# Kernel optimization log

Hardware: AMD Instinct MI355X
Metric: run time of the kernel (lower is better)

The kernel has to match this reference:

```python
import jax, jax.numpy as jnp
import numpy as np

B, C, T = 128, 9, 2048
R = T // 4            # reduced_timesteps after two MaxPool1d(2)
N = B * R             # total graph nodes
E_SINGLE = 8192       # edges per sample graph (avg degree 16 over R nodes)
HID = 128
OUT = 12


def setup_inputs():
    key = jax.random.key(0)
    ks = jax.random.split(key, 14)
    x = jax.random.normal(ks[0], (B, C, T), jnp.float32)
    # per-sample graph, replicated with offset i*R per batch element (as in forward)
    single = jax.random.randint(ks[1], (2, E_SINGLE), 0, R)
    offsets = (jnp.arange(B) * R)[None, :, None]
    edge_index = (single[:, None, :] + offsets).reshape(2, -1)  # [2, B*E_SINGLE]

    def lin(k, fan_in, shape):
        return jax.random.normal(k, shape, jnp.float32) / np.sqrt(fan_in)

    return {
        "x": x,
        "edge_index": edge_index,
        "conv1_w": lin(ks[2], C * 5, (16, C, 5)),
        "conv1_b": jnp.zeros((16,), jnp.float32),
        "conv2_w": lin(ks[3], 16 * 5, (32, 16, 5)),
        "conv2_b": jnp.zeros((32,), jnp.float32),
        "gcn1_w": lin(ks[4], 32, (32, HID)),
        "gcn1_b": jnp.zeros((HID,), jnp.float32),
        "gcn2_w": lin(ks[5], HID, (HID, HID)),
        "gcn2_b": jnp.zeros((HID,), jnp.float32),
        "fc_w": lin(ks[6], HID, (HID, OUT)),
        "fc_b": jnp.zeros((OUT,), jnp.float32),
    }


def _gcn_conv(h, edge_index, w, b, n):
    # PyG GCNConv: linear -> add self-loops -> sym-normalized sum aggregation -> + bias
    h = h @ w
    loops = jnp.arange(n)
    row = jnp.concatenate([edge_index[0], loops])  # source
    col = jnp.concatenate([edge_index[1], loops])  # target (aggregation)
    deg = jax.ops.segment_sum(jnp.ones(col.shape, h.dtype), col, num_segments=n)
    dis = jnp.where(deg > 0, jax.lax.rsqrt(jnp.maximum(deg, 1e-12)), 0.0)
    norm = dis[row] * dis[col]                      # [E+N]
    out = jax.ops.segment_sum(norm[:, None] * h[row], col, num_segments=n)
    return out + b


def _temporal_conv(x, w1, b1, w2, b2):
    dn = ("NCH", "OIH", "NCH")
    h = jax.lax.conv_general_dilated(x, w1, (1,), [(2, 2)], dimension_numbers=dn)
    h = jax.nn.relu(h + b1[None, :, None])
    h = jax.lax.reduce_window(h, -jnp.inf, jax.lax.max, (1, 1, 2), (1, 1, 2), "VALID")
    h = jax.lax.conv_general_dilated(h, w2, (1,), [(2, 2)], dimension_numbers=dn)
    h = jax.nn.relu(h + b2[None, :, None])
    h = jax.lax.reduce_window(h, -jnp.inf, jax.lax.max, (1, 1, 2), (1, 1, 2), "VALID")
    return h  # [B, 32, R]


def reference(x, edge_index, conv1_w, conv1_b, conv2_w, conv2_b,
              gcn1_w, gcn1_b, gcn2_w, gcn2_b, fc_w, fc_b):
    h = _temporal_conv(x, conv1_w, conv1_b, conv2_w, conv2_b)   # [B, 32, R]
    nodes = h.transpose(0, 2, 1).reshape(B * R, 32)             # [N, 32]
    g = jax.nn.relu(_gcn_conv(nodes, edge_index, gcn1_w, gcn1_b, N))
    g = jax.nn.relu(_gcn_conv(g, edge_index, gcn2_w, gcn2_b, N))
    g = g.reshape(B, R, HID).mean(axis=1)                       # [B, HID]
    return g @ fc_w + fc_b                                      # [B, OUT]
```

## Files before the change

kernel.cpp:

```cpp
#include <hip/hip_runtime.h>
#include <hip/hip_bf16.h>

#define BB   128
#define CIN  9
#define TT   2048
#define RR   512
#define NN   (BB*RR)
#define HID  128
#define NOUT 12

typedef __attribute__((ext_vector_type(8))) short short8;
typedef __attribute__((ext_vector_type(4))) float f32x4;

static __device__ inline unsigned short f2bf(float f) {
    unsigned int u = __float_as_uint(f);
    unsigned int r = (u + 0x7fffu + ((u >> 16) & 1u)) >> 16;
    return (unsigned short)r;
}
static __device__ inline float bf2f(unsigned short u) {
    return __uint_as_float(((unsigned int)u) << 16);
}

__global__ __launch_bounds__(512) void k_convs(const float* __restrict__ x,
        const float* __restrict__ w1, const float* __restrict__ b1,
        const float* __restrict__ w2, const float* __restrict__ b2,
        float* __restrict__ nodes,
        const int* __restrict__ ei, int E, int es,
        int* __restrict__ rptr, float* __restrict__ dis, int* __restrict__ adj) {
    __shared__ float sx[CIN][268];
    __shared__ float s1[16][132];
    __shared__ int lcnt[512];
    __shared__ int sp[512];
    __shared__ int lcur[512];
    int tid = threadIdx.x;

    if (blockIdx.x == 1024) {
        int t = tid;
        lcnt[t] = 0;
        __syncthreads();
        for (int i = t; i < es; i += 512) atomicAdd(&lcnt[ei[E + i]], 1);
        __syncthreads();
        int c = lcnt[t];
        sp[t] = c;
        __syncthreads();
        for (int off = 1; off < 512; off <<= 1) {
            int v = sp[t];
            int add = (t >= off) ? sp[t - off] : 0;
            __syncthreads();
            sp[t] = v + add;
            __syncthreads();
        }
        int excl = sp[t] - c;
        rptr[t] = excl;
        if (t == 511) rptr[512] = es;
        dis[t] = rsqrtf((float)c + 1.0f);
        lcur[t] = excl;
        __syncthreads();
        for (int i = t; i < es; i += 512) {
            int row = ei[i], col = ei[E + i];
            int pos = atomicAdd(&lcur[col], 1);
            adj[pos] = row;
        }
        return;
    }

    int b  = blockIdx.x >> 3;
    int r0 = (blockIdx.x & 7) * 64;
    int wv   = __builtin_amdgcn_readfirstlane(tid >> 6);
    int lane = tid & 63;

    for (int idx = tid; idx < CIN * 268; idx += 512) {
        int c = idx / 268, j = idx - c * 268;
        int g = 4 * r0 - 6 + j;
        float v = 0.f;
        if (g >= 0 && g < TT) v = x[(b * CIN + c) * TT + g];
        sx[c][j] = v;
    }
    __syncthreads();

#pragma unroll
    for (int cc = 0; cc < 2; ++cc) {
        int c1 = wv * 2 + cc;
        float bias1 = b1[c1];
        for (int pp = lane; pp < 132; pp += 64) {
            int p = 2 * r0 - 2 + pp;
            float val = 0.f;
            if (p >= 0 && p < 1024) {
                float a0 = bias1, a1 = bias1;
#pragma unroll
                for (int c = 0; c < CIN; ++c) {
                    const float2* px = (const float2*)&sx[c][2 * pp];
                    float2 q0 = px[0], q1 = px[1], q2 = px[2];
                    const float* wp = &w1[(c1 * CIN + c) * 5];
                    float k0 = wp[0], k1 = wp[1], k2 = wp[2], k3 = wp[3], k4 = wp[4];
                    a0 += q0.x*k0 + q0.y*k1 + q1.x*k2 + q1.y*k3 + q2.x*k4;
                    a1 += q0.y*k0 + q1.x*k1 + q1.y*k2 + q2.x*k3 + q2.y*k4;
                }
                val = fmaxf(fmaxf(a0, a1), 0.f);
            }
            s1[c1][pp] = val;
        }
    }
    __syncthreads();

    int rl = lane;
    float acc0[4], acc1[4];
#pragma unroll
    for (int o = 0; o < 4; ++o) {
        float bv = b2[wv * 4 + o];
        acc0[o] = bv; acc1[o] = bv;
    }
#pragma unroll
    for (int c = 0; c < 16; ++c) {
        const float2* ps = (const float2*)&s1[c][2 * rl];
        float2 q0 = ps[0], q1 = ps[1], q2 = ps[2];
#pragma unroll
        for (int o = 0; o < 4; ++o) {
            const float* wp = &w2[((wv * 4 + o) * 16 + c) * 5];
            float k0 = wp[0], k1 = wp[1], k2 = wp[2], k3 = wp[3], k4 = wp[4];
            acc0[o] += q0.x*k0 + q0.y*k1 + q1.x*k2 + q1.y*k3 + q2.x*k4;
            acc1[o] += q0.y*k0 + q1.x*k1 + q1.y*k2 + q2.x*k3 + q2.y*k4;
        }
    }
    int n = b * RR + r0 + rl;
    float4 ov;
    ov.x = fmaxf(fmaxf(acc0[0], acc1[0]), 0.f);
    ov.y = fmaxf(fmaxf(acc0[1], acc1[1]), 0.f);
    ov.z = fmaxf(fmaxf(acc0[2], acc1[2]), 0.f);
    ov.w = fmaxf(fmaxf(acc0[3], acc1[3]), 0.f);
    *(float4*)&nodes[n * 32 + wv * 4] = ov;
}

__global__ __launch_bounds__(256) void k_gl1(const int* __restrict__ rptr,
        const int* __restrict__ adj, const float* __restrict__ dis,
        const float* __restrict__ nodes, const float* __restrict__ w,
        const float* __restrict__ bias, unsigned short* __restrict__ h16) {
    __shared__ float srow[32][32];
    __shared__ float sw[32 * 128];
    int bid = (blockIdx.x & 7) * 256 + (blockIdx.x >> 3);
    int tid = threadIdx.x;
    int nbase = bid * 32;
    int b = nbase >> 9;
    const float* hb = nodes + (size_t)b * RR * 32;

    {
        const float4* src = (const float4*)w;
        float4* dst = (float4*)sw;
#pragma unroll
        for (int i = 0; i < 4; ++i) dst[tid + i * 256] = src[tid + i * 256];
    }

    int ln   = tid >> 3;
    int lane = tid & 7;
    int r = (nbase & 511) + ln;
    int s = rptr[r], e = rptr[r + 1];
    float dn = dis[r];
    float4 acc = make_float4(0.f, 0.f, 0.f, 0.f);
    for (int base = s; base < e; base += 8) {
        int j = base + lane;
        int src = 0; float nd = 0.f;
        if (j < e) { src = adj[j]; nd = dis[src]; }
        int cnt = min(8, e - base);
        int k = 0;
        for (; k + 4 <= cnt; k += 4) {
            int   s0 = __shfl(src, k, 8),     s1 = __shfl(src, k + 1, 8);
            int   s2 = __shfl(src, k + 2, 8), s3 = __shfl(src, k + 3, 8);
            float n0 = __shfl(nd, k, 8),      n1 = __shfl(nd, k + 1, 8);
            float n2 = __shfl(nd, k + 2, 8),  n3 = __shfl(nd, k + 3, 8);
            float4 v0 = *(const float4*)&hb[(size_t)s0 * 32 + lane * 4];
            float4 v1 = *(const float4*)&hb[(size_t)s1 * 32 + lane * 4];
            float4 v2 = *(const float4*)&hb[(size_t)s2 * 32 + lane * 4];
            float4 v3 = *(const float4*)&hb[(size_t)s3 * 32 + lane * 4];
            float w0 = dn * n0, w1 = dn * n1, w2 = dn * n2, w3 = dn * n3;
            acc.x += w0*v0.x + w1*v1.x + w2*v2.x + w3*v3.x;
            acc.y += w0*v0.y + w1*v1.y + w2*v2.y + w3*v3.y;
            acc.z += w0*v0.z + w1*v1.z + w2*v2.z + w3*v3.z;
            acc.w += w0*v0.w + w1*v1.w + w2*v2.w + w3*v3.w;
        }
        for (; k < cnt; ++k) {
            int   sk = __shfl(src, k, 8);
            float nk = __shfl(nd, k, 8);
            float4 v = *(const float4*)&hb[(size_t)sk * 32 + lane * 4];
            float wgt = dn * nk;
            acc.x += wgt * v.x; acc.y += wgt * v.y;
            acc.z += wgt * v.z; acc.w += wgt * v.w;
        }
    }
    {
        float4 v = *(const float4*)&hb[(size_t)r * 32 + lane * 4];
        float wgt = dn * dn;
        acc.x += wgt * v.x; acc.y += wgt * v.y;
        acc.z += wgt * v.z; acc.w += wgt * v.w;
    }
    *(float4*)&srow[ln][lane * 4] = acc;
    __syncthreads();

    int fq = tid & 31;
    int ng = tid >> 5;
    float a[4][4];
#pragma unroll
    for (int j = 0; j < 4; ++j)
#pragma unroll
        for (int q = 0; q < 4; ++q) a[j][q] = 0.f;
#pragma unroll
    for (int c = 0; c < 32; ++c) {
        float4 wvv = *(const float4*)&sw[c * 128 + fq * 4];
#pragma unroll
        for (int j = 0; j < 4; ++j) {
            float xc = srow[ng * 4 + j][c];
            a[j][0] += xc * wvv.x; a[j][1] += xc * wvv.y;
            a[j][2] += xc * wvv.z; a[j][3] += xc * wvv.w;
        }
    }
    float4 bv = *(const float4*)&bias[fq * 4];
#pragma unroll
    for (int j = 0; j < 4; ++j) {
        ushort4 o;
        o.x = f2bf(fmaxf(a[j][0] + bv.x, 0.f));
        o.y = f2bf(fmaxf(a[j][1] + bv.y, 0.f));
        o.z = f2bf(fmaxf(a[j][2] + bv.z, 0.f));
        o.w = f2bf(fmaxf(a[j][3] + bv.w, 0.f));
        *(ushort4*)&h16[(size_t)(nbase + ng * 4 + j) * 128 + fq * 4] = o;
    }
}

__global__ __launch_bounds__(256) void k_lin2(const unsigned short* __restrict__ g16,
        const float* __restrict__ w, unsigned short* __restrict__ h16) {
    __shared__ unsigned short srow[64][136];
    __shared__ unsigned short swT[128][136];
    int tid = threadIdx.x;
    int nbase = blockIdx.x * 64;

    {
        const ushort4* src = (const ushort4*)(g16 + (size_t)nbase * 128);
#pragma unroll
        for (int i = 0; i < 8; ++i) {
            int idx = tid + i * 256;
            int row = idx >> 5, col4 = idx & 31;
            ushort4 v = src[idx];
            *(ushort4*)&srow[row][col4 * 4] = v;
        }
    }
    {
        for (int i = 0; i < 64; ++i) {
            int idx = i * 256 + tid;
            int c = idx >> 7, f = idx & 127;
            swT[f][c] = f2bf(w[idx]);
        }
    }
    __syncthreads();

    int wv  = tid >> 6;
    int lane = tid & 63;
    int m0 = wv * 16;
    int l15 = lane & 15;
    int quad = lane >> 4;
    f32x4 acc[8];
#pragma unroll
    for (int nt = 0; nt < 8; ++nt) acc[nt] = (f32x4){0.f, 0.f, 0.f, 0.f};
#pragma unroll
    for (int kc = 0; kc < 4; ++kc) {
        int k0 = kc * 32 + quad * 8;
        short8 a = *(const short8*)&srow[m0 + l15][k0];
#pragma unroll
        for (int nt = 0; nt < 8; ++nt) {
            short8 b = *(const short8*)&swT[nt * 16 + l15][k0];
            acc[nt] = __builtin_amdgcn_mfma_f32_16x16x32_bf16(a, b, acc[nt], 0, 0, 0);
        }
    }
#pragma unroll
    for (int nt = 0; nt < 8; ++nt) {
#pragma unroll
        for (int r = 0; r < 4; ++r) {
            int row = m0 + quad * 4 + r;
            int col = nt * 16 + l15;
            h16[(size_t)(nbase + row) * 128 + col] = f2bf(acc[nt][r]);
        }
    }
}

__global__ __launch_bounds__(256) void k_gather128(const int* __restrict__ rptr,
        const int* __restrict__ adj, const float* __restrict__ dis,
        const unsigned short* __restrict__ h, const float* __restrict__ bias,
        float* __restrict__ partial) {
    __shared__ float sred[8][128];
    int bid  = (blockIdx.x & 7) * 1024 + (blockIdx.x >> 3);
    int tid  = threadIdx.x;
    int g    = tid >> 5;
    int lane = tid & 31;
    int node = bid * 8 + g;
    int b = node >> 9;
    int r = node & 511;
    const unsigned short* hb = h + (size_t)b * RR * 128;
    int s = rptr[r], e = rptr[r + 1];
    float dn = dis[r];
    float4 acc = make_float4(0.f, 0.f, 0.f, 0.f);
    for (int base = s; base < e; base += 32) {
        int j = base + lane;
        int src = 0; float nd = 0.f;
        if (j < e) { src = adj[j]; nd = dis[src]; }
        int cnt = min(32, e - base);
        int k = 0;
        for (; k + 4 <= cnt; k += 4) {
            int   s0 = __shfl(src, k, 32),     s1 = __shfl(src, k + 1, 32);
            int   s2 = __shfl(src, k + 2, 32), s3 = __shfl(src, k + 3, 32);
            float n0 = __shfl(nd, k, 32),      n1 = __shfl(nd, k + 1, 32);
            float n2 = __shfl(nd, k + 2, 32),  n3 = __shfl(nd, k + 3, 32);
            ushort4 u0 = *(const ushort4*)&hb[(size_t)s0 * 128 + lane * 4];
            ushort4 u1 = *(const ushort4*)&hb[(size_t)s1 * 128 + lane * 4];
            ushort4 u2 = *(const ushort4*)&hb[(size_t)s2 * 128 + lane * 4];
            ushort4 u3 = *(const ushort4*)&hb[(size_t)s3 * 128 + lane * 4];
            float w0 = dn * n0, w1 = dn * n1, w2 = dn * n2, w3 = dn * n3;
            acc.x += w0*bf2f(u0.x) + w1*bf2f(u1.x) + w2*bf2f(u2.x) + w3*bf2f(u3.x);
            acc.y += w0*bf2f(u0.y) + w1*bf2f(u1.y) + w2*bf2f(u2.y) + w3*bf2f(u3.y);
            acc.z += w0*bf2f(u0.z) + w1*bf2f(u1.z) + w2*bf2f(u2.z) + w3*bf2f(u3.z);
            acc.w += w0*bf2f(u0.w) + w1*bf2f(u1.w) + w2*bf2f(u2.w) + w3*bf2f(u3.w);
        }
        for (; k < cnt; ++k) {
            int   sk = __shfl(src, k, 32);
            float nk = __shfl(nd, k, 32);
            ushort4 u = *(const ushort4*)&hb[(size_t)sk * 128 + lane * 4];
            float wgt = dn * nk;
            acc.x += wgt * bf2f(u.x); acc.y += wgt * bf2f(u.y);
            acc.z += wgt * bf2f(u.z); acc.w += wgt * bf2f(u.w);
        }
    }
    ushort4 u = *(const ushort4*)&hb[(size_t)r * 128 + lane * 4];
    float wgt = dn * dn;
    float4 bv = *(const float4*)&bias[lane * 4];
    acc.x = fmaxf(acc.x + wgt * bf2f(u.x) + bv.x, 0.f);
    acc.y = fmaxf(acc.y + wgt * bf2f(u.y) + bv.y, 0.f);
    acc.z = fmaxf(acc.z + wgt * bf2f(u.z) + bv.z, 0.f);
    acc.w = fmaxf(acc.w + wgt * bf2f(u.w) + bv.w, 0.f);
    *(float4*)&sred[g][lane * 4] = acc;
    __syncthreads();
    if (tid < 128) {
        float ssum = 0.f;
#pragma unroll
        for (int j = 0; j < 8; ++j) ssum += sred[j][tid];
        partial[(size_t)bid * 128 + tid] = ssum;
    }
}

__global__ __launch_bounds__(128) void k_fc(const float* __restrict__ partial,
        const float* __restrict__ fw, const float* __restrict__ fb,
        float* __restrict__ out) {
    __shared__ float sm[HID];
    int b = blockIdx.x, f = threadIdx.x;
    float acc = 0.f;
#pragma unroll 8
    for (int j = 0; j < 64; ++j) acc += partial[(size_t)(b * 64 + j) * 128 + f];
    sm[f] = acc * (1.0f / RR);
    __syncthreads();
    if (f < NOUT) {
        float s = fb[f];
#pragma unroll
        for (int c = 0; c < HID; ++c) s += sm[c] * fw[c * NOUT + f];
        out[b * NOUT + f] = s;
    }
}

extern "C" void kernel_launch(void* const* d_in, const int* in_sizes, int n_in,
                              void* d_out, int out_size, void* d_ws, size_t ws_size,
                              hipStream_t stream) {
    const float* x   = (const float*)d_in[0];
    const int*   ei  = (const int*)d_in[1];
    const float* c1w = (const float*)d_in[2];
    const float* c1b = (const float*)d_in[3];
    const float* c2w = (const float*)d_in[4];
    const float* c2b = (const float*)d_in[5];
    const float* g1w = (const float*)d_in[6];
    const float* g1b = (const float*)d_in[7];
    const float* g2w = (const float*)d_in[8];
    const float* g2b = (const float*)d_in[9];
    const float* fw  = (const float*)d_in[10];
    const float* fb  = (const float*)d_in[11];
    float* out = (float*)d_out;
    int E  = in_sizes[1] / 2;
    int es = E / BB;

    char* ws = (char*)d_ws;
    float*          nodes   = (float*)(ws);
    unsigned short* bufA16  = (unsigned short*)(ws + (8u  << 20));
    unsigned short* bufC16  = (unsigned short*)(ws + (24u << 20));
    int*   rptr    = (int*)  (ws + (40u << 20));
    float* dis     = (float*)(ws + (40u << 20) + 4096);
    int*   adj     = (int*)  (ws + (40u << 20) + 8192);
    float* partial = (float*)(ws + (41u << 20));

    k_convs<<<BB * 8 + 1, 512, 0, stream>>>(x, c1w, c1b, c2w, c2b, nodes,
                                            ei, E, es, rptr, dis, adj);

    k_gl1<<<NN / 32, 256, 0, stream>>>(rptr, adj, dis, nodes, g1w, g1b, bufA16);

    k_lin2<<<NN / 64, 256, 0, stream>>>(bufA16, g2w, bufC16);
    k_gather128<<<NN / 8, 256, 0, stream>>>(rptr, adj, dis, bufC16, g2b, partial);

    k_fc<<<BB, 128, 0, stream>>>(partial, fw, fb, out);
}
```

Before: 176.0 us.

## Stage per-sample graph in LDS, fuse layer-2 linear with gather, use MFMA

```diff
diff --git a/kernel.cpp b/kernel.cpp
--- a/kernel.cpp
+++ b/kernel.cpp
@@ -26,7 +26,9 @@
         const float* __restrict__ w2, const float* __restrict__ b2,
         float* __restrict__ nodes,
         const int* __restrict__ ei, int E, int es,
-        int* __restrict__ rptr, float* __restrict__ dis, int* __restrict__ adj) {
+        int* __restrict__ rptr, float* __restrict__ dis, int* __restrict__ adj,
+        const float* __restrict__ g1w, const float* __restrict__ g2w,
+        unsigned short* __restrict__ w1t, unsigned short* __restrict__ w2t) {
     __shared__ float sx[CIN][268];
     __shared__ float s1[16][132];
     __shared__ int lcnt[512];
@@ -63,6 +65,17 @@
         }
         return;
     }
+    if (blockIdx.x == 1025) {
+        for (int idx = tid; idx < 32 * 128; idx += 512) {
+            int c = idx >> 7, f = idx & 127;
+            w1t[f * 32 + c] = f2bf(g1w[idx]);
+        }
+        for (int idx = tid; idx < 128 * 128; idx += 512) {
+            int c = idx >> 7, f = idx & 127;
+            w2t[f * 128 + c] = f2bf(g2w[idx]);
+        }
+        return;
+    }
 
     int b  = blockIdx.x >> 3;
     int r0 = (blockIdx.x & 7) * 64;
@@ -131,214 +144,226 @@
     *(float4*)&nodes[n * 32 + wv * 4] = ov;
 }
 
-__global__ __launch_bounds__(256) void k_gl1(const int* __restrict__ rptr,
+__global__ __launch_bounds__(512, 2) void k_gl1(const int* __restrict__ rptr,
         const int* __restrict__ adj, const float* __restrict__ dis,
-        const float* __restrict__ nodes, const float* __restrict__ w,
+        const float* __restrict__ nodes, const unsigned short* __restrict__ w1t,
         const float* __restrict__ bias, unsigned short* __restrict__ h16) {
-    __shared__ float srow[32][32];
-    __shared__ float sw[32 * 128];
-    int bid = (blockIdx.x & 7) * 256 + (blockIdx.x >> 3);
+    __shared__ float snode[512][36];
+    __shared__ unsigned short srow[256][40];
+    __shared__ float sdis[512];
     int tid = threadIdx.x;
-    int nbase = bid * 32;
-    int b = nbase >> 9;
-    const float* hb = nodes + (size_t)b * RR * 32;
+    int vb = blockIdx.x;
+    int xcd = vb & 7, slot = vb >> 3;
+    int b = xcd * 16 + (slot >> 1);
+    int half = slot & 1;
 
     {
-        const float4* src = (const float4*)w;
-        float4* dst = (float4*)sw;
-#pragma unroll
-        for (int i = 0; i < 4; ++i) dst[tid + i * 256] = src[tid + i * 256];
-    }
-
-    int ln   = tid >> 3;
-    int lane = tid & 7;
-    int r = (nbase & 511) + ln;
-    int s = rptr[r], e = rptr[r + 1];
-    float dn = dis[r];
-    float4 acc = make_float4(0.f, 0.f, 0.f, 0.f);
-    for (int base = s; base < e; base += 8) {
-        int j = base + lane;
-        int src = 0; float nd = 0.f;
-        if (j < e) { src = adj[j]; nd = dis[src]; }
-        int cnt = min(8, e - base);
-        int k = 0;
-        for (; k + 4 <= cnt; k += 4) {
-            int   s0 = __shfl(src, k, 8),     s1 = __shfl(src, k + 1, 8);
-            int   s2 = __shfl(src, k + 2, 8), s3 = __shfl(src, k + 3, 8);
-            float n0 = __shfl(nd, k, 8),      n1 = __shfl(nd, k + 1, 8);
-            float n2 = __shfl(nd, k + 2, 8),  n3 = __shfl(nd, k + 3, 8);
-            float4 v0 = *(const float4*)&hb[(size_t)s0 * 32 + lane * 4];
-            float4 v1 = *(const float4*)&hb[(size_t)s1 * 32 + lane * 4];
-            float4 v2 = *(const float4*)&hb[(size_t)s2 * 32 + lane * 4];
-            float4 v3 = *(const float4*)&hb[(size_t)s3 * 32 + lane * 4];
-            float w0 = dn * n0, w1 = dn * n1, w2 = dn * n2, w3 = dn * n3;
-            acc.x += w0*v0.x + w1*v1.x + w2*v2.x + w3*v3.x;
-            acc.y += w0*v0.y + w1*v1.y + w2*v2.y + w3*v3.y;
-            acc.z += w0*v0.z + w1*v1.z + w2*v2.z + w3*v3.z;
-            acc.w += w0*v0.w + w1*v1.w + w2*v2.w + w3*v3.w;
-        }
-        for (; k < cnt; ++k) {
-            int   sk = __shfl(src, k, 8);
-            float nk = __shfl(nd, k, 8);
-            float4 v = *(const float4*)&hb[(size_t)sk * 32 + lane * 4];
-            float wgt = dn * nk;
+        const float4* src = (const float4*)(nodes + (size_t)b * RR * 32);
+#pragma unroll
+        for (int i = 0; i < 32; ++i) {
+            int idx = tid + i * 512;
+            int row = idx >> 3, c4 = idx & 7;
+            *(float4*)&snode[row][c4 * 4] = src[idx];
+        }
+        if (tid < 512) sdis[tid] = dis[tid];
+    }
+    __syncthreads();
+
+    int lane8 = tid & 7;
+    int gidx  = tid >> 3;
+#pragma unroll
+    for (int nlg = 0; nlg < 4; ++nlg) {
+        int nl = nlg * 64 + gidx;
+        int r  = half * 256 + nl;
+        int s = rptr[r], e = rptr[r + 1];
+        float dn = sdis[r];
+        float4 acc = make_float4(0.f, 0.f, 0.f, 0.f);
+        for (int base = s; base < e; base += 8) {
+            int j = base + lane8;
+            int src = 0; float nd = 0.f;
+            if (j < e) { src = adj[j]; nd = sdis[src]; }
+            int cnt = min(8, e - base);
+            int k = 0;
+            for (; k + 4 <= cnt; k += 4) {
+                int   s0 = __shfl(src, k, 8),     s1 = __shfl(src, k + 1, 8);
+                int   s2 = __shfl(src, k + 2, 8), s3 = __shfl(src, k + 3, 8);
+                float n0 = __shfl(nd, k, 8),      n1 = __shfl(nd, k + 1, 8);
+                float n2 = __shfl(nd, k + 2, 8),  n3 = __shfl(nd, k + 3, 8);
+                float4 v0 = *(const float4*)&snode[s0][lane8 * 4];
+                float4 v1 = *(const float4*)&snode[s1][lane8 * 4];
+                float4 v2 = *(const float4*)&snode[s2][lane8 * 4];
+                float4 v3 = *(const float4*)&snode[s3][lane8 * 4];
+                float w0 = dn * n0, w1 = dn * n1, w2 = dn * n2, w3 = dn * n3;
+                acc.x += w0*v0.x + w1*v1.x + w2*v2.x + w3*v3.x;
+                acc.y += w0*v0.y + w1*v1.y + w2*v2.y + w3*v3.y;
+                acc.z += w0*v0.z + w1*v1.z + w2*v2.z + w3*v3.z;
+                acc.w += w0*v0.w + w1*v1.w + w2*v2.w + w3*v3.w;
+            }
+            for (; k < cnt; ++k) {
+                int   sk = __shfl(src, k, 8);
+                float nk = __shfl(nd, k, 8);
+                float4 v = *(const float4*)&snode[sk][lane8 * 4];
+                float wgt = dn * nk;
+                acc.x += wgt * v.x; acc.y += wgt * v.y;
+                acc.z += wgt * v.z; acc.w += wgt * v.w;
+            }
+        }
+        {
+            float4 v = *(const float4*)&snode[r][lane8 * 4];
+            float wgt = dn * dn;
             acc.x += wgt * v.x; acc.y += wgt * v.y;
             acc.z += wgt * v.z; acc.w += wgt * v.w;
         }
-    }
+        ushort4 o;
+        o.x = f2bf(acc.x); o.y = f2bf(acc.y); o.z = f2bf(acc.z); o.w = f2bf(acc.w);
+        *(ushort4*)&srow[nl][lane8 * 4] = o;
+    }
+    __syncthreads();
+
+    int wv   = tid >> 6;
+    int lane = tid & 63;
+    int l15  = lane & 15;
+    int quad = lane >> 4;
+    short8 bfr[8];
+#pragma unroll
+    for (int nt = 0; nt < 8; ++nt)
+        bfr[nt] = *(const short8*)&w1t[(nt * 16 + l15) * 32 + quad * 8];
+    float bcol[8];
+#pragma unroll
+    for (int nt = 0; nt < 8; ++nt) bcol[nt] = bias[nt * 16 + l15];
+#pragma unroll
+    for (int t = 0; t < 2; ++t) {
+        int m0 = wv * 32 + t * 16;
+        short8 a = *(const short8*)&srow[m0 + l15][quad * 8];
+        f32x4 acc[8];
+#pragma unroll
+        for (int nt = 0; nt < 8; ++nt) {
+            acc[nt] = (f32x4){0.f, 0.f, 0.f, 0.f};
+            acc[nt] = __builtin_amdgcn_mfma_f32_16x16x32_bf16(a, bfr[nt], acc[nt], 0, 0, 0);
+        }
+#pragma unroll
+        for (int nt = 0; nt < 8; ++nt) {
+            int col = nt * 16 + l15;
+#pragma unroll
+            for (int rr2 = 0; rr2 < 4; ++rr2) {
+                int node = b * RR + half * 256 + m0 + quad * 4 + rr2;
+                h16[(size_t)node * 128 + col] = f2bf(fmaxf(acc[nt][rr2] + bcol[nt], 0.f));
+            }
+        }
+    }
+}
+
+__global__ __launch_bounds__(512, 2) void k_l2(const int* __restrict__ rptr,
+        const int* __restrict__ adj, const float* __restrict__ dis,
+        const unsigned short* __restrict__ h1, const unsigned short* __restrict__ w2t,
+        const float* __restrict__ bias, float* __restrict__ partial) {
+    __shared__ unsigned short hwin[512][136];
+    __shared__ float sgrp[16][128];
+    __shared__ float sdis[512];
+    int tid = threadIdx.x;
+    int vb = blockIdx.x;
+    int xcd = vb & 7, slot = vb >> 3;
+    int b = xcd * 16 + (slot >> 1);
+    int half = slot & 1;
+
     {
-        float4 v = *(const float4*)&hb[(size_t)r * 32 + lane * 4];
+        const ushort4* src = (const ushort4*)(h1 + (size_t)b * RR * 128);
+#pragma unroll
+        for (int i = 0; i < 32; ++i) {
+            int idx = tid + i * 512;
+            int row = idx >> 5, c4 = idx & 31;
+            *(ushort4*)&hwin[row][c4 * 4] = src[idx];
+        }
+        if (tid < 512) sdis[tid] = dis[tid];
+    }
+    __syncthreads();
+
+    int wv   = tid >> 6;
+    int lane = tid & 63;
+    int l15  = lane & 15;
+    int quad = lane >> 4;
+    short8 bfr[8][4];
+#pragma unroll
+    for (int nt = 0; nt < 8; ++nt)
+#pragma unroll
+        for (int kc = 0; kc < 4; ++kc)
+            bfr[nt][kc] = *(const short8*)&w2t[(nt * 16 + l15) * 128 + kc * 32 + quad * 8];
+#pragma unroll
+    for (int mt = 0; mt < 4; ++mt) {
+        int m0 = wv * 64 + mt * 16;
+        short8 a[4];
+#pragma unroll
+        for (int kc = 0; kc < 4; ++kc)
+            a[kc] = *(const short8*)&hwin[m0 + l15][kc * 32 + quad * 8];
+        f32x4 acc[8];
+#pragma unroll
+        for (int nt = 0; nt < 8; ++nt) acc[nt] = (f32x4){0.f, 0.f, 0.f, 0.f};
+#pragma unroll
+        for (int kc = 0; kc < 4; ++kc)
+#pragma unroll
+            for (int nt = 0; nt < 8; ++nt)
+                acc[nt] = __builtin_amdgcn_mfma_f32_16x16x32_bf16(a[kc], bfr[nt][kc], acc[nt], 0, 0, 0);
+#pragma unroll
+        for (int nt = 0; nt < 8; ++nt)
+#pragma unroll
+            for (int rr2 = 0; rr2 < 4; ++rr2)
+                hwin[m0 + quad * 4 + rr2][nt * 16 + l15] = f2bf(acc[nt][rr2]);
+    }
+    __syncthreads();
+
+    int grp   = tid >> 5;
+    int lane32 = tid & 31;
+    float4 bv = *(const float4*)&bias[lane32 * 4];
+    float4 csum = make_float4(0.f, 0.f, 0.f, 0.f);
+    for (int ni = 0; ni < 16; ++ni) {
+        int r = half * 256 + grp * 16 + ni;
+        int s = rptr[r], e = rptr[r + 1];
+        float dn = sdis[r];
+        float4 acc = make_float4(0.f, 0.f, 0.f, 0.f);
+        for (int base = s; base < e; base += 32) {
+            int j = base + lane32;
+            int src = 0; float nd = 0.f;
+            if (j < e) { src = adj[j]; nd = sdis[src]; }
+            int cnt = min(32, e - base);
+            int k = 0;
+            for (; k + 4 <= cnt; k += 4) {
+                int   s0 = __shfl(src, k, 32),     s1 = __shfl(src, k + 1, 32);
+                int   s2 = __shfl(src, k + 2, 32), s3 = __shfl(src, k + 3, 32);
+                float n0 = __shfl(nd, k, 32),      n1 = __shfl(nd, k + 1, 32);
+                float n2 = __shfl(nd, k + 2, 32),  n3 = __shfl(nd, k + 3, 32);
+                ushort4 u0 = *(const ushort4*)&hwin[s0][lane32 * 4];
+                ushort4 u1 = *(const ushort4*)&hwin[s1][lane32 * 4];
+                ushort4 u2 = *(const ushort4*)&hwin[s2][lane32 * 4];
+                ushort4 u3 = *(const ushort4*)&hwin[s3][lane32 * 4];
+                float w0 = dn * n0, w1 = dn * n1, w2 = dn * n2, w3 = dn * n3;
+                acc.x += w0*bf2f(u0.x) + w1*bf2f(u1.x) + w2*bf2f(u2.x) + w3*bf2f(u3.x);
+                acc.y += w0*bf2f(u0.y) + w1*bf2f(u1.y) + w2*bf2f(u2.y) + w3*bf2f(u3.y);
+                acc.z += w0*bf2f(u0.z) + w1*bf2f(u1.z) + w2*bf2f(u2.z) + w3*bf2f(u3.z);
+                acc.w += w0*bf2f(u0.w) + w1*bf2f(u1.w) + w2*bf2f(u2.w) + w3*bf2f(u3.w);
+            }
+            for (; k < cnt; ++k) {
+                int   sk = __shfl(src, k, 32);
+                float nk = __shfl(nd, k, 32);
+                ushort4 u = *(const ushort4*)&hwin[sk][lane32 * 4];
+                float wgt = dn * nk;
+                acc.x += wgt * bf2f(u.x); acc.y += wgt * bf2f(u.y);
+                acc.z += wgt * bf2f(u.z); acc.w += wgt * bf2f(u.w);
+            }
+        }
+        ushort4 u = *(const ushort4*)&hwin[r][lane32 * 4];
         float wgt = dn * dn;
-        acc.x += wgt * v.x; acc.y += wgt * v.y;
-        acc.z += wgt * v.z; acc.w += wgt * v.w;
-    }
-    *(float4*)&srow[ln][lane * 4] = acc;
-    __syncthreads();
-
-    int fq = tid & 31;
-    int ng = tid >> 5;
-    float a[4][4];
-#pragma unroll
-    for (int j = 0; j < 4; ++j)
-#pragma unroll
-        for (int q = 0; q < 4; ++q) a[j][q] = 0.f;
-#pragma unroll
-    for (int c = 0; c < 32; ++c) {
-        float4 wvv = *(const float4*)&sw[c * 128 + fq * 4];
-#pragma unroll
-        for (int j = 0; j < 4; ++j) {
-            float xc = srow[ng * 4 + j][c];
-            a[j][0] += xc * wvv.x; a[j][1] += xc * wvv.y;
-            a[j][2] += xc * wvv.z; a[j][3] += xc * wvv.w;
-        }
-    }
-    float4 bv = *(const float4*)&bias[fq * 4];
-#pragma unroll
-    for (int j = 0; j < 4; ++j) {
-        ushort4 o;
-        o.x = f2bf(fmaxf(a[j][0] + bv.x, 0.f));
-        o.y = f2bf(fmaxf(a[j][1] + bv.y, 0.f));
-        o.z = f2bf(fmaxf(a[j][2] + bv.z, 0.f));
-        o.w = f2bf(fmaxf(a[j][3] + bv.w, 0.f));
-        *(ushort4*)&h16[(size_t)(nbase + ng * 4 + j) * 128 + fq * 4] = o;
-    }
-}
-
-__global__ __launch_bounds__(256) void k_lin2(const unsigned short* __restrict__ g16,
-        const float* __restrict__ w, unsigned short* __restrict__ h16) {
-    __shared__ unsigned short srow[64][136];
-    __shared__ unsigned short swT[128][136];
-    int tid = threadIdx.x;
-    int nbase = blockIdx.x * 64;
-
-    {
-        const ushort4* src = (const ushort4*)(g16 + (size_t)nbase * 128);
-#pragma unroll
-        for (int i = 0; i < 8; ++i) {
-            int idx = tid + i * 256;
-            int row = idx >> 5, col4 = idx & 31;
-            ushort4 v = src[idx];
-            *(ushort4*)&srow[row][col4 * 4] = v;
-        }
-    }
-    {
-        for (int i = 0; i < 64; ++i) {
-            int idx = i * 256 + tid;
-            int c = idx >> 7, f = idx & 127;
-            swT[f][c] = f2bf(w[idx]);
-        }
-    }
-    __syncthreads();
-
-    int wv  = tid >> 6;
-    int lane = tid & 63;
-    int m0 = wv * 16;
-    int l15 = lane & 15;
-    int quad = lane >> 4;
-    f32x4 acc[8];
-#pragma unroll
-    for (int nt = 0; nt < 8; ++nt) acc[nt] = (f32x4){0.f, 0.f, 0.f, 0.f};
-#pragma unroll
-    for (int kc = 0; kc < 4; ++kc) {
-        int k0 = kc * 32 + quad * 8;
-        short8 a = *(const short8*)&srow[m0 + l15][k0];
-#pragma unroll
-        for (int nt = 0; nt < 8; ++nt) {
-            short8 b = *(const short8*)&swT[nt * 16 + l15][k0];
-            acc[nt] = __builtin_amdgcn_mfma_f32_16x16x32_bf16(a, b, acc[nt], 0, 0, 0);
-        }
-    }
-#pragma unroll
-    for (int nt = 0; nt < 8; ++nt) {
-#pragma unroll
-        for (int r = 0; r < 4; ++r) {
-            int row = m0 + quad * 4 + r;
-            int col = nt * 16 + l15;
-            h16[(size_t)(nbase + row) * 128 + col] = f2bf(acc[nt][r]);
-        }
-    }
-}
-
-__global__ __launch_bounds__(256) void k_gather128(const int* __restrict__ rptr,
-        const int* __restrict__ adj, const float* __restrict__ dis,
-        const unsigned short* __restrict__ h, const float* __restrict__ bias,
-        float* __restrict__ partial) {
-    __shared__ float sred[8][128];
-    int bid  = (blockIdx.x & 7) * 1024 + (blockIdx.x >> 3);
-    int tid  = threadIdx.x;
-    int g    = tid >> 5;
-    int lane = tid & 31;
-    int node = bid * 8 + g;
-    int b = node >> 9;
-    int r = node & 511;
-    const unsigned short* hb = h + (size_t)b * RR * 128;
-    int s = rptr[r], e = rptr[r + 1];
-    float dn = dis[r];
-    float4 acc = make_float4(0.f, 0.f, 0.f, 0.f);
-    for (int base = s; base < e; base += 32) {
-        int j = base + lane;
-        int src = 0; float nd = 0.f;
-        if (j < e) { src = adj[j]; nd = dis[src]; }
-        int cnt = min(32, e - base);
-        int k = 0;
-        for (; k + 4 <= cnt; k += 4) {
-            int   s0 = __shfl(src, k, 32),     s1 = __shfl(src, k + 1, 32);
-            int   s2 = __shfl(src, k + 2, 32), s3 = __shfl(src, k + 3, 32);
-            float n0 = __shfl(nd, k, 32),      n1 = __shfl(nd, k + 1, 32);
-            float n2 = __shfl(nd, k + 2, 32),  n3 = __shfl(nd, k + 3, 32);
-            ushort4 u0 = *(const ushort4*)&hb[(size_t)s0 * 128 + lane * 4];
-            ushort4 u1 = *(const ushort4*)&hb[(size_t)s1 * 128 + lane * 4];
-            ushort4 u2 = *(const ushort4*)&hb[(size_t)s2 * 128 + lane * 4];
-            ushort4 u3 = *(const ushort4*)&hb[(size_t)s3 * 128 + lane * 4];
-            float w0 = dn * n0, w1 = dn * n1, w2 = dn * n2, w3 = dn * n3;
-            acc.x += w0*bf2f(u0.x) + w1*bf2f(u1.x) + w2*bf2f(u2.x) + w3*bf2f(u3.x);
-            acc.y += w0*bf2f(u0.y) + w1*bf2f(u1.y) + w2*bf2f(u2.y) + w3*bf2f(u3.y);
-            acc.z += w0*bf2f(u0.z) + w1*bf2f(u1.z) + w2*bf2f(u2.z) + w3*bf2f(u3.z);
-            acc.w += w0*bf2f(u0.w) + w1*bf2f(u1.w) + w2*bf2f(u2.w) + w3*bf2f(u3.w);
-        }
-        for (; k < cnt; ++k) {
-            int   sk = __shfl(src, k, 32);
-            float nk = __shfl(nd, k, 32);
-            ushort4 u = *(const ushort4*)&hb[(size_t)sk * 128 + lane * 4];
-            float wgt = dn * nk;
-            acc.x += wgt * bf2f(u.x); acc.y += wgt * bf2f(u.y);
-            acc.z += wgt * bf2f(u.z); acc.w += wgt * bf2f(u.w);
-        }
-    }
-    ushort4 u = *(const ushort4*)&hb[(size_t)r * 128 + lane * 4];
-    float wgt = dn * dn;
-    float4 bv = *(const float4*)&bias[lane * 4];
-    acc.x = fmaxf(acc.x + wgt * bf2f(u.x) + bv.x, 0.f);
-    acc.y = fmaxf(acc.y + wgt * bf2f(u.y) + bv.y, 0.f);
-    acc.z = fmaxf(acc.z + wgt * bf2f(u.z) + bv.z, 0.f);
-    acc.w = fmaxf(acc.w + wgt * bf2f(u.w) + bv.w, 0.f);
-    *(float4*)&sred[g][lane * 4] = acc;
+        csum.x += fmaxf(acc.x + wgt * bf2f(u.x) + bv.x, 0.f);
+        csum.y += fmaxf(acc.y + wgt * bf2f(u.y) + bv.y, 0.f);
+        csum.z += fmaxf(acc.z + wgt * bf2f(u.z) + bv.z, 0.f);
+        csum.w += fmaxf(acc.w + wgt * bf2f(u.w) + bv.w, 0.f);
+    }
+    *(float4*)&sgrp[grp][lane32 * 4] = csum;
     __syncthreads();
     if (tid < 128) {
         float ssum = 0.f;
 #pragma unroll
-        for (int j = 0; j < 8; ++j) ssum += sred[j][tid];
-        partial[(size_t)bid * 128 + tid] = ssum;
+        for (int j = 0; j < 16; ++j) ssum += sgrp[j][tid];
+        partial[(size_t)(b * 2 + half) * 128 + tid] = ssum;
     }
 }
 
@@ -347,9 +372,7 @@
         float* __restrict__ out) {
     __shared__ float sm[HID];
     int b = blockIdx.x, f = threadIdx.x;
-    float acc = 0.f;
-#pragma unroll 8
-    for (int j = 0; j < 64; ++j) acc += partial[(size_t)(b * 64 + j) * 128 + f];
+    float acc = partial[(size_t)(b * 2) * 128 + f] + partial[(size_t)(b * 2 + 1) * 128 + f];
     sm[f] = acc * (1.0f / RR);
     __syncthreads();
     if (f < NOUT) {
@@ -382,19 +405,20 @@
     char* ws = (char*)d_ws;
     float*          nodes   = (float*)(ws);
     unsigned short* bufA16  = (unsigned short*)(ws + (8u  << 20));
-    unsigned short* bufC16  = (unsigned short*)(ws + (24u << 20));
-    int*   rptr    = (int*)  (ws + (40u << 20));
-    float* dis     = (float*)(ws + (40u << 20) + 4096);
-    int*   adj     = (int*)  (ws + (40u << 20) + 8192);
-    float* partial = (float*)(ws + (41u << 20));
-
-    k_convs<<<BB * 8 + 1, 512, 0, stream>>>(x, c1w, c1b, c2w, c2b, nodes,
-                                            ei, E, es, rptr, dis, adj);
-
-    k_gl1<<<NN / 32, 256, 0, stream>>>(rptr, adj, dis, nodes, g1w, g1b, bufA16);
-
-    k_lin2<<<NN / 64, 256, 0, stream>>>(bufA16, g2w, bufC16);
-    k_gather128<<<NN / 8, 256, 0, stream>>>(rptr, adj, dis, bufC16, g2b, partial);
+    int*   rptr    = (int*)  (ws + (24u << 20));
+    float* dis     = (float*)(ws + (24u << 20) + 4096);
+    int*   adj     = (int*)  (ws + (24u << 20) + 8192);
+    unsigned short* w1t = (unsigned short*)(ws + (24u << 20) + 49152);
+    unsigned short* w2t = (unsigned short*)(ws + (24u << 20) + 65536);
+    float* partial = (float*)(ws + (25u << 20));
+
+    k_convs<<<1026, 512, 0, stream>>>(x, c1w, c1b, c2w, c2b, nodes,
+                                      ei, E, es, rptr, dis, adj,
+                                      g1w, g2w, w1t, w2t);
+
+    k_gl1<<<256, 512, 0, stream>>>(rptr, adj, dis, nodes, w1t, g1b, bufA16);
+
+    k_l2<<<256, 512, 0, stream>>>(rptr, adj, dis, bufA16, w2t, g2b, partial);
 
     k_fc<<<BB, 128, 0, stream>>>(partial, fw, fb, out);
 }
```

Result: no change. 178.8 us (+1.6%).

## Pack edge source and degree norm, widen gather waves, restructure conv tiling

Applied to the files above, without the earlier changes.

```diff
diff --git a/kernel.cpp b/kernel.cpp
--- a/kernel.cpp
+++ b/kernel.cpp
@@ -26,15 +26,17 @@
         const float* __restrict__ w2, const float* __restrict__ b2,
         float* __restrict__ nodes,
         const int* __restrict__ ei, int E, int es,
-        int* __restrict__ rptr, float* __restrict__ dis, int* __restrict__ adj) {
-    __shared__ float sx[CIN][268];
-    __shared__ float s1[16][132];
-    __shared__ int lcnt[512];
-    __shared__ int sp[512];
-    __shared__ int lcur[512];
+        int* __restrict__ rptr, float* __restrict__ dis,
+        int* __restrict__ adj, int2* __restrict__ edat) {
+    __shared__ float sx[CIN][524];
+    __shared__ float s1[16][260];
+    __shared__ int   lcnt[512];
+    __shared__ int   sp[512];
+    __shared__ int   lcur[512];
+    __shared__ float sdisl[512];
     int tid = threadIdx.x;
 
-    if (blockIdx.x == 1024) {
+    if (blockIdx.x == 512) {
         int t = tid;
         lcnt[t] = 0;
         __syncthreads();
@@ -53,24 +55,25 @@
         int excl = sp[t] - c;
         rptr[t] = excl;
         if (t == 511) rptr[512] = es;
-        dis[t] = rsqrtf((float)c + 1.0f);
+        float dv = rsqrtf((float)c + 1.0f);
+        dis[t] = dv;
+        sdisl[t] = dv;
         lcur[t] = excl;
         __syncthreads();
         for (int i = t; i < es; i += 512) {
             int row = ei[i], col = ei[E + i];
             int pos = atomicAdd(&lcur[col], 1);
             adj[pos] = row;
+            edat[pos] = make_int2(row, __float_as_int(sdisl[row]));
         }
         return;
     }
 
-    int b  = blockIdx.x >> 3;
-    int r0 = (blockIdx.x & 7) * 64;
-    int wv   = __builtin_amdgcn_readfirstlane(tid >> 6);
-    int lane = tid & 63;
-
-    for (int idx = tid; idx < CIN * 268; idx += 512) {
-        int c = idx / 268, j = idx - c * 268;
+    int b  = blockIdx.x >> 2;
+    int r0 = (blockIdx.x & 3) * 128;
+
+    for (int idx = tid; idx < CIN * 524; idx += 512) {
+        int c = idx / 524, j = idx - c * 524;
         int g = 4 * r0 - 6 + j;
         float v = 0.f;
         if (g >= 0 && g < TT) v = x[(b * CIN + c) * TT + g];
@@ -78,57 +81,62 @@
     }
     __syncthreads();
 
-#pragma unroll
-    for (int cc = 0; cc < 2; ++cc) {
-        int c1 = wv * 2 + cc;
-        float bias1 = b1[c1];
-        for (int pp = lane; pp < 132; pp += 64) {
-            int p = 2 * r0 - 2 + pp;
-            float val = 0.f;
-            if (p >= 0 && p < 1024) {
-                float a0 = bias1, a1 = bias1;
-#pragma unroll
-                for (int c = 0; c < CIN; ++c) {
-                    const float2* px = (const float2*)&sx[c][2 * pp];
-                    float2 q0 = px[0], q1 = px[1], q2 = px[2];
-                    const float* wp = &w1[(c1 * CIN + c) * 5];
+    if (tid < 260) {
+        int pp = tid;
+        int p  = 2 * r0 - 2 + pp;
+        float a0[16], a1[16];
+        bool valid = (p >= 0 && p < 1024);
+#pragma unroll
+        for (int o = 0; o < 16; ++o) { float bv = b1[o]; a0[o] = bv; a1[o] = bv; }
+        if (valid) {
+#pragma unroll
+            for (int c = 0; c < CIN; ++c) {
+                float xv0 = sx[c][2*pp+0], xv1 = sx[c][2*pp+1], xv2 = sx[c][2*pp+2];
+                float xv3 = sx[c][2*pp+3], xv4 = sx[c][2*pp+4], xv5 = sx[c][2*pp+5];
+#pragma unroll
+                for (int o = 0; o < 16; ++o) {
+                    const float* wp = &w1[(o * CIN + c) * 5];
                     float k0 = wp[0], k1 = wp[1], k2 = wp[2], k3 = wp[3], k4 = wp[4];
-                    a0 += q0.x*k0 + q0.y*k1 + q1.x*k2 + q1.y*k3 + q2.x*k4;
-                    a1 += q0.y*k0 + q1.x*k1 + q1.y*k2 + q2.x*k3 + q2.y*k4;
+                    a0[o] += xv0*k0 + xv1*k1 + xv2*k2 + xv3*k3 + xv4*k4;
+                    a1[o] += xv1*k0 + xv2*k1 + xv3*k2 + xv4*k3 + xv5*k4;
                 }
-                val = fmaxf(fmaxf(a0, a1), 0.f);
             }
-            s1[c1][pp] = val;
-        }
-    }
-    __syncthreads();
-
-    int rl = lane;
-    float acc0[4], acc1[4];
-#pragma unroll
-    for (int o = 0; o < 4; ++o) {
-        float bv = b2[wv * 4 + o];
-        acc0[o] = bv; acc1[o] = bv;
-    }
+        }
+#pragma unroll
+        for (int o = 0; o < 16; ++o)
+            s1[o][pp] = valid ? fmaxf(fmaxf(a0[o], a1[o]), 0.f) : 0.f;
+    }
+    __syncthreads();
+
+    int rl = tid & 127;
+    int g  = __builtin_amdgcn_readfirstlane(tid >> 7);
+    float c0[8], c1v[8];
+#pragma unroll
+    for (int o = 0; o < 8; ++o) { float bv = b2[g * 8 + o]; c0[o] = bv; c1v[o] = bv; }
 #pragma unroll
     for (int c = 0; c < 16; ++c) {
-        const float2* ps = (const float2*)&s1[c][2 * rl];
-        float2 q0 = ps[0], q1 = ps[1], q2 = ps[2];
-#pragma unroll
-        for (int o = 0; o < 4; ++o) {
-            const float* wp = &w2[((wv * 4 + o) * 16 + c) * 5];
+        float xv0 = s1[c][2*rl+0], xv1 = s1[c][2*rl+1], xv2 = s1[c][2*rl+2];
+        float xv3 = s1[c][2*rl+3], xv4 = s1[c][2*rl+4], xv5 = s1[c][2*rl+5];
+#pragma unroll
+        for (int o = 0; o < 8; ++o) {
+            const float* wp = &w2[((g * 8 + o) * 16 + c) * 5];
             float k0 = wp[0], k1 = wp[1], k2 = wp[2], k3 = wp[3], k4 = wp[4];
-            acc0[o] += q0.x*k0 + q0.y*k1 + q1.x*k2 + q1.y*k3 + q2.x*k4;
-            acc1[o] += q0.y*k0 + q1.x*k1 + q1.y*k2 + q2.x*k3 + q2.y*k4;
+            c0[o]  += xv0*k0 + xv1*k1 + xv2*k2 + xv3*k3 + xv4*k4;
+            c1v[o] += xv1*k0 + xv2*k1 + xv3*k2 + xv4*k3 + xv5*k4;
         }
     }
     int n = b * RR + r0 + rl;
-    float4 ov;
-    ov.x = fmaxf(fmaxf(acc0[0], acc1[0]), 0.f);
-    ov.y = fmaxf(fmaxf(acc0[1], acc1[1]), 0.f);
-    ov.z = fmaxf(fmaxf(acc0[2], acc1[2]), 0.f);
-    ov.w = fmaxf(fmaxf(acc0[3], acc1[3]), 0.f);
-    *(float4*)&nodes[n * 32 + wv * 4] = ov;
+    float4 ova, ovb;
+    ova.x = fmaxf(fmaxf(c0[0], c1v[0]), 0.f);
+    ova.y = fmaxf(fmaxf(c0[1], c1v[1]), 0.f);
+    ova.z = fmaxf(fmaxf(c0[2], c1v[2]), 0.f);
+    ova.w = fmaxf(fmaxf(c0[3], c1v[3]), 0.f);
+    ovb.x = fmaxf(fmaxf(c0[4], c1v[4]), 0.f);
+    ovb.y = fmaxf(fmaxf(c0[5], c1v[5]), 0.f);
+    ovb.z = fmaxf(fmaxf(c0[6], c1v[6]), 0.f);
+    ovb.w = fmaxf(fmaxf(c0[7], c1v[7]), 0.f);
+    *(float4*)&nodes[n * 32 + g * 8]     = ova;
+    *(float4*)&nodes[n * 32 + g * 8 + 4] = ovb;
 }
 
 __global__ __launch_bounds__(256) void k_gl1(const int* __restrict__ rptr,
@@ -279,60 +287,55 @@
     }
 }
 
-__global__ __launch_bounds__(256) void k_gather128(const int* __restrict__ rptr,
-        const int* __restrict__ adj, const float* __restrict__ dis,
+__global__ __launch_bounds__(512) void k_g128(const int* __restrict__ rptr,
+        const int2* __restrict__ edat, const float* __restrict__ dis,
         const unsigned short* __restrict__ h, const float* __restrict__ bias,
         float* __restrict__ partial) {
     __shared__ float sred[8][128];
+    int tid  = threadIdx.x;
     int bid  = (blockIdx.x & 7) * 1024 + (blockIdx.x >> 3);
-    int tid  = threadIdx.x;
-    int g    = tid >> 5;
-    int lane = tid & 31;
-    int node = bid * 8 + g;
+    int wv   = __builtin_amdgcn_readfirstlane(tid >> 6);
+    int lane = tid & 63;
+    int node = bid * 8 + wv;
     int b = node >> 9;
     int r = node & 511;
     const unsigned short* hb = h + (size_t)b * RR * 128;
     int s = rptr[r], e = rptr[r + 1];
     float dn = dis[r];
-    float4 acc = make_float4(0.f, 0.f, 0.f, 0.f);
-    for (int base = s; base < e; base += 32) {
-        int j = base + lane;
-        int src = 0; float nd = 0.f;
-        if (j < e) { src = adj[j]; nd = dis[src]; }
-        int cnt = min(32, e - base);
-        int k = 0;
-        for (; k + 4 <= cnt; k += 4) {
-            int   s0 = __shfl(src, k, 32),     s1 = __shfl(src, k + 1, 32);
-            int   s2 = __shfl(src, k + 2, 32), s3 = __shfl(src, k + 3, 32);
-            float n0 = __shfl(nd, k, 32),      n1 = __shfl(nd, k + 1, 32);
-            float n2 = __shfl(nd, k + 2, 32),  n3 = __shfl(nd, k + 3, 32);
-            ushort4 u0 = *(const ushort4*)&hb[(size_t)s0 * 128 + lane * 4];
-            ushort4 u1 = *(const ushort4*)&hb[(size_t)s1 * 128 + lane * 4];
-            ushort4 u2 = *(const ushort4*)&hb[(size_t)s2 * 128 + lane * 4];
-            ushort4 u3 = *(const ushort4*)&hb[(size_t)s3 * 128 + lane * 4];
-            float w0 = dn * n0, w1 = dn * n1, w2 = dn * n2, w3 = dn * n3;
-            acc.x += w0*bf2f(u0.x) + w1*bf2f(u1.x) + w2*bf2f(u2.x) + w3*bf2f(u3.x);
-            acc.y += w0*bf2f(u0.y) + w1*bf2f(u1.y) + w2*bf2f(u2.y) + w3*bf2f(u3.y);
-            acc.z += w0*bf2f(u0.z) + w1*bf2f(u1.z) + w2*bf2f(u2.z) + w3*bf2f(u3.z);
-            acc.w += w0*bf2f(u0.w) + w1*bf2f(u1.w) + w2*bf2f(u2.w) + w3*bf2f(u3.w);
-        }
-        for (; k < cnt; ++k) {
-            int   sk = __shfl(src, k, 32);
-            float nk = __shfl(nd, k, 32);
-            ushort4 u = *(const ushort4*)&hb[(size_t)sk * 128 + lane * 4];
-            float wgt = dn * nk;
-            acc.x += wgt * bf2f(u.x); acc.y += wgt * bf2f(u.y);
-            acc.z += wgt * bf2f(u.z); acc.w += wgt * bf2f(u.w);
-        }
-    }
-    ushort4 u = *(const ushort4*)&hb[(size_t)r * 128 + lane * 4];
-    float wgt = dn * dn;
-    float4 bv = *(const float4*)&bias[lane * 4];
-    acc.x = fmaxf(acc.x + wgt * bf2f(u.x) + bv.x, 0.f);
-    acc.y = fmaxf(acc.y + wgt * bf2f(u.y) + bv.y, 0.f);
-    acc.z = fmaxf(acc.z + wgt * bf2f(u.z) + bv.z, 0.f);
-    acc.w = fmaxf(acc.w + wgt * bf2f(u.w) + bv.w, 0.f);
-    *(float4*)&sred[g][lane * 4] = acc;
+    float a0 = 0.f, a1 = 0.f;
+    int k = s;
+    for (; k + 4 <= e; k += 4) {
+        int2 p0 = edat[k],     p1 = edat[k + 1];
+        int2 p2 = edat[k + 2], p3 = edat[k + 3];
+        unsigned int u0 = *(const unsigned int*)&hb[(size_t)p0.x * 128 + lane * 2];
+        unsigned int u1 = *(const unsigned int*)&hb[(size_t)p1.x * 128 + lane * 2];
+        unsigned int u2 = *(const unsigned int*)&hb[(size_t)p2.x * 128 + lane * 2];
+        unsigned int u3 = *(const unsigned int*)&hb[(size_t)p3.x * 128 + lane * 2];
+        float w0 = __int_as_float(p0.y), w1 = __int_as_float(p1.y);
+        float w2 = __int_as_float(p2.y), w3 = __int_as_float(p3.y);
+        a0 += w0 * bf2f((unsigned short)(u0 & 0xffff))
+            + w1 * bf2f((unsigned short)(u1 & 0xffff))
+            + w2 * bf2f((unsigned short)(u2 & 0xffff))
+            + w3 * bf2f((unsigned short)(u3 & 0xffff));
+        a1 += w0 * bf2f((unsigned short)(u0 >> 16))
+            + w1 * bf2f((unsigned short)(u1 >> 16))
+            + w2 * bf2f((unsigned short)(u2 >> 16))
+            + w3 * bf2f((unsigned short)(u3 >> 16));
+    }
+    for (; k < e; ++k) {
+        int2 p = edat[k];
+        unsigned int u = *(const unsigned int*)&hb[(size_t)p.x * 128 + lane * 2];
+        float w = __int_as_float(p.y);
+        a0 += w * bf2f((unsigned short)(u & 0xffff));
+        a1 += w * bf2f((unsigned short)(u >> 16));
+    }
+    unsigned int us = *(const unsigned int*)&hb[(size_t)r * 128 + lane * 2];
+    float2 bv = *(const float2*)&bias[lane * 2];
+    float dn2 = dn * dn;
+    float o0 = fmaxf(dn * a0 + dn2 * bf2f((unsigned short)(us & 0xffff)) + bv.x, 0.f);
+    float o1 = fmaxf(dn * a1 + dn2 * bf2f((unsigned short)(us >> 16)) + bv.y, 0.f);
+    sred[wv][lane * 2]     = o0;
+    sred[wv][lane * 2 + 1] = o1;
     __syncthreads();
     if (tid < 128) {
         float ssum = 0.f;
@@ -386,15 +389,16 @@
     int*   rptr    = (int*)  (ws + (40u << 20));
     float* dis     = (float*)(ws + (40u << 20) + 4096);
     int*   adj     = (int*)  (ws + (40u << 20) + 8192);
+    int2*  edat    = (int2*) (ws + (40u << 20) + 65536);
     float* partial = (float*)(ws + (41u << 20));
 
-    k_convs<<<BB * 8 + 1, 512, 0, stream>>>(x, c1w, c1b, c2w, c2b, nodes,
-                                            ei, E, es, rptr, dis, adj);
+    k_convs<<<513, 512, 0, stream>>>(x, c1w, c1b, c2w, c2b, nodes,
+                                     ei, E, es, rptr, dis, adj, edat);
 
     k_gl1<<<NN / 32, 256, 0, stream>>>(rptr, adj, dis, nodes, g1w, g1b, bufA16);
 
     k_lin2<<<NN / 64, 256, 0, stream>>>(bufA16, g2w, bufC16);
-    k_gather128<<<NN / 8, 256, 0, stream>>>(rptr, adj, dis, bufC16, g2b, partial);
+    k_g128<<<NN / 8, 512, 0, stream>>>(rptr, edat, dis, bufC16, g2b, partial);
 
     k_fc<<<BB, 128, 0, stream>>>(partial, fw, fb, out);
 }
```

Result: slower. 397.3 us (+125.7%).
